# Kernel tuning notes

Hardware: AMD Instinct MI355X
Metric: run time of the kernel (lower is better)

The kernel has to match this reference:

```python
import jax, jax.numpy as jnp
import numpy as np

B, HG, WG, D, NH, K = 4, 32, 32, 768, 12, 7
HD = D // NH  # 64


def _neigh_idx(H, W, k):
    # NATTEN semantics: 7x7 window centered at the query, shifted (clamped)
    # at borders so every query has exactly k*k neighbors.
    si = np.clip(np.arange(H) - k // 2, 0, H - k)  # [H] window row starts
    sj = np.clip(np.arange(W) - k // 2, 0, W - k)  # [W] window col starts
    ri = si[:, None] + np.arange(k)[None, :]       # [H, k]
    cj = sj[:, None] + np.arange(k)[None, :]       # [W, k]
    idx = ri[:, None, :, None] * W + cj[None, :, None, :]  # [H, W, k, k]
    return jnp.asarray(idx.reshape(H * W, k * k), dtype=jnp.int32)


def setup_inputs() -> dict:
    key = jax.random.key(0)
    ks = jax.random.split(key, 3)
    s = D ** -0.5
    return {
        "x": jax.random.normal(ks[0], (B, HG * WG, D), dtype=jnp.float32),
        "qkv_w": jax.random.normal(ks[1], (3 * D, D), dtype=jnp.float32) * s,
        "qkv_b": jnp.zeros((3 * D,), dtype=jnp.float32),
        "proj_w": jax.random.normal(ks[2], (D, D), dtype=jnp.float32) * s,
        "proj_b": jnp.zeros((D,), dtype=jnp.float32),
    }


def reference(x, qkv_w, qkv_b, proj_w, proj_b):
    b, n, d = x.shape  # n == HG*WG
    idx = _neigh_idx(HG, WG, K)  # [n, K*K] flat neighbor token indices

    qkv = x @ qkv_w.T + qkv_b                      # [b, n, 3d]
    q, k, v = jnp.split(qkv, 3, axis=-1)
    q = q.reshape(b, n, NH, HD) * (HD ** -0.5)     # [b, n, h, hd]
    k = k.reshape(b, n, NH, HD)
    v = v.reshape(b, n, NH, HD)

    kn = jnp.take(k, idx, axis=1)                  # [b, n, 49, h, hd]
    vn = jnp.take(v, idx, axis=1)                  # [b, n, 49, h, hd]

    scores = jnp.einsum('bnhd,bnkhd->bnhk', q, kn)  # [b, n, h, 49]
    attn = jax.nn.softmax(scores, axis=-1)
    out = jnp.einsum('bnhk,bnkhd->bnhd', attn, vn).reshape(b, n, d)
    return out @ proj_w.T + proj_b
```

## Files before the change

### kernel.cpp

```cpp
#include <hip/hip_runtime.h>


typedef __bf16 bf16x8 __attribute__((ext_vector_type(8)));
typedef short s16x4 __attribute__((ext_vector_type(4)));
typedef float f32x4 __attribute__((ext_vector_type(4)));

__device__ __forceinline__ unsigned short f2bf(float f) {
  unsigned u = __float_as_uint(f);
  u += 0x7fffu + ((u >> 16) & 1u);
  return (unsigned short)(u >> 16);
}

template <typename T>
__device__ __forceinline__ void gld_lds16(const T* g, T* l) {
  __builtin_amdgcn_global_load_lds((const __attribute__((address_space(1))) void*)g,
                                   (__attribute__((address_space(3))) void*)l, 16, 0, 0);
}

__global__ void cvt_kernel(const float* __restrict__ x, const float* __restrict__ w1,
                           const float* __restrict__ w2, unsigned short* __restrict__ xo,
                           unsigned short* __restrict__ w1o, unsigned short* __restrict__ w2o) {
  const int n1 = 4096 * 768 / 4;
  const int n2 = 2304 * 768 / 4;
  const int n3 = 768 * 768 / 4;
  int i = blockIdx.x * 256 + threadIdx.x;
  float4 v;
  unsigned short* dst;
  int o;
  if (i < n1) {
    o = i; v = ((const float4*)x)[o]; dst = xo;
  } else if (i < n1 + n2) {
    o = i - n1; v = ((const float4*)w1)[o]; dst = w1o;
  } else if (i < n1 + n2 + n3) {
    o = i - n1 - n2; v = ((const float4*)w2)[o]; dst = w2o;
  } else {
    return;
  }
  ushort4 r;
  r.x = f2bf(v.x); r.y = f2bf(v.y); r.z = f2bf(v.z); r.w = f2bf(v.w);
  ((ushort4*)dst)[o] = r;
}

template <int NT, int MODE>
__global__ __launch_bounds__(256) void gemm_bt(const unsigned short* __restrict__ A,
                                               const unsigned short* __restrict__ Bm,
                                               const float* __restrict__ bias,
                                               unsigned short* __restrict__ obf,
                                               unsigned short* __restrict__ vtout,
                                               float* __restrict__ of32,
                                               int N) {
  constexpr int KD = 768;
  constexpr int SBW = NT / 2;
  __shared__ __align__(16) unsigned short sA[64 * 32];
  __shared__ __align__(16) unsigned short sB[NT * 32 * 32];
  const int tid = threadIdx.x, lane = tid & 63, wv = tid >> 6;
  const int lr = lane & 15, lq = lane >> 4;
  const int m0 = blockIdx.y * 64;
  const int n0 = blockIdx.x * (NT * 32);

  const unsigned short* pA = A + (size_t)(m0 + wv * 16 + lr) * KD + lq * 8;
  const unsigned short* pB[SBW];
#pragma unroll
  for (int j = 0; j < SBW; ++j)
    pB[j] = Bm + (size_t)(n0 + (wv * SBW + j) * 16 + lr) * KD + lq * 8;

  f32x4 acc[2][NT] = {};

  for (int k0 = 0; k0 < KD; k0 += 32) {
    gld_lds16(pA + k0, sA + tid * 8);
#pragma unroll
    for (int j = 0; j < SBW; ++j)
      gld_lds16(pB[j] + k0, sB + (wv * SBW + j) * 512 + lane * 8);
    __syncthreads();

    bf16x8 af[2], bfb[NT];
#pragma unroll
    for (int im = 0; im < 2; ++im)
      af[im] = *(const bf16x8*)(sA + ((wv >> 1) * 2 + im) * 512 + lq * 128 + lr * 8);
#pragma unroll
    for (int in = 0; in < NT; ++in)
      bfb[in] = *(const bf16x8*)(sB + ((wv & 1) * NT + in) * 512 + lq * 128 + lr * 8);
#pragma unroll
    for (int im = 0; im < 2; ++im)
#pragma unroll
      for (int in = 0; in < NT; ++in)
        acc[im][in] = __builtin_amdgcn_mfma_f32_16x16x32_bf16(af[im], bfb[in], acc[im][in], 0, 0, 0);
    __syncthreads();
  }

  const int mw = m0 + (wv >> 1) * 32;
  const int nw = n0 + (wv & 1) * (NT * 16);
#pragma unroll
  for (int im = 0; im < 2; ++im) {
#pragma unroll
    for (int in = 0; in < NT; ++in) {
      int gn = nw + in * 16 + lr;
      float bsv = bias[gn];
      if (MODE == 0) {
        int sidx = gn / 768;
        int rem = gn - sidx * 768;
        int hh = rem >> 6, dd = gn & 63;
        if (sidx == 2) {
          int gm0 = mw + im * 16 + lq * 4;
          ushort4 pk;
          pk.x = f2bf(acc[im][in][0] + bsv);
          pk.y = f2bf(acc[im][in][1] + bsv);
          pk.z = f2bf(acc[im][in][2] + bsv);
          pk.w = f2bf(acc[im][in][3] + bsv);
          *(ushort4*)(vtout + (size_t)(hh * 64 + dd) * 4096 + gm0) = pk;
        } else {
          const float scale = (sidx == 0) ? 0.18033688f : 1.0f;
#pragma unroll
          for (int r = 0; r < 4; ++r) {
            int gm = mw + im * 16 + lq * 4 + r;
            obf[((size_t)(sidx * 12 + hh) * 4096 + gm) * 64 + dd] = f2bf((acc[im][in][r] + bsv) * scale);
          }
        }
      } else {
#pragma unroll
        for (int r = 0; r < 4; ++r) {
          int gm = mw + im * 16 + lq * 4 + r;
          of32[(size_t)gm * N + gn] = acc[im][in][r] + bsv;
        }
      }
    }
  }
}

__global__ __launch_bounds__(256, 2) void natten_kernel(const unsigned short* __restrict__ qkvt,
                                                        unsigned short* __restrict__ aout) {
  __shared__ __align__(16) unsigned short sQ[64 * 64];
  __shared__ __align__(16) unsigned short sK[256 * 64];
  __shared__ __align__(16) unsigned short sVt[64 * 256];
  const int h = blockIdx.x, ip = blockIdx.y, b = blockIdx.z;
  const int i0 = ip * 2;
  const int tid = threadIdx.x, lane = tid & 63, wv = tid >> 6;
  const int lg = lane >> 4, lm = lane & 15;
  int si0 = i0 - 3; si0 = si0 < 0 ? 0 : si0; if (si0 > 25) si0 = 25;
  const int gb = b * 1024;
  const unsigned short* Qg = qkvt + ((size_t)h * 4096 + gb + i0 * 32) * 64;
  const unsigned short* Kg = qkvt + ((size_t)(12 + h) * 4096 + gb) * 64;
  const unsigned short* Vg = qkvt + (size_t)24 * 4096 * 64 + (size_t)h * 64 * 4096 + gb;

#pragma unroll
  for (int it = 0; it < 2; ++it) {
    int f = it * 256 + tid;
    int q = f >> 3, c16 = f & 7;
    uint4 v = *(const uint4*)(Qg + q * 64 + c16 * 8);
    int s = q & 15;
    *(uint2*)(sQ + q * 64 + ((((c16 << 1)) ^ s) << 2)) = make_uint2(v.x, v.y);
    *(uint2*)(sQ + q * 64 + ((((c16 << 1) | 1) ^ s) << 2)) = make_uint2(v.z, v.w);
  }
#pragma unroll
  for (int it = 0; it < 8; ++it) {
    int f = it * 256 + tid;
    int t = f >> 3, c16 = f & 7;
    int wr = t >> 5, c = t & 31;
    int row = si0 + wr; if (row > 31) row = 31;
    uint4 v = *(const uint4*)(Kg + (row * 32 + c) * 64 + c16 * 8);
    int s = t & 15;
    *(uint2*)(sK + t * 64 + ((((c16 << 1)) ^ s) << 2)) = make_uint2(v.x, v.y);
    *(uint2*)(sK + t * 64 + ((((c16 << 1) | 1) ^ s) << 2)) = make_uint2(v.z, v.w);
  }
#pragma unroll
  for (int it = 0; it < 8; ++it) {
    int f = it * 256 + tid;
    int d = f >> 5, tc16 = f & 31;
    int wr = tc16 >> 2;
    int row = si0 + wr; if (row > 31) row = 31;
    uint4 v = *(const uint4*)(Vg + (size_t)d * 4096 + row * 32 + (tc16 & 3) * 8);
    int s = d & 15;
    *(uint2*)(sVt + d * 256 + ((((tc16 << 1)) ^ s) << 2)) = make_uint2(v.x, v.y);
    *(uint2*)(sVt + d * 256 + ((((tc16 << 1) | 1) ^ s) << 2)) = make_uint2(v.z, v.w);
  }
  __syncthreads();

  const int row_sel = wv >> 1;
  const int jhalf = wv & 1;
  const int i = i0 + row_sel;
  int si_w = i - 3; si_w = si_w < 0 ? 0 : si_w; if (si_w > 25) si_w = 25;
  const int toff = (si_w - si0) * 32;
  const int j = jhalf * 16 + lm;
  int sj = j - 3; sj = sj < 0 ? 0 : sj; if (sj > 25) sj = 25;

  float madd[2][4];
#pragma unroll
  for (int p = 0; p < 2; ++p)
#pragma unroll
    for (int r = 0; r < 4; ++r) {
      int c = p * 16 + lg * 4 + r;
      madd[p][r] = (c >= sj && c <= sj + 6) ? 0.f : -1e30f;
    }

  s16x4 qf[4];
  const int qrow = row_sel * 32 + j;
#pragma unroll
  for (int ks = 0; ks < 4; ++ks)
    qf[ks] = *(const s16x4*)(sQ + qrow * 64 + ((((ks << 2) + lg) ^ (qrow & 15)) << 2));

  f32x4 accS[14];
#pragma unroll
  for (int tt = 0; tt < 14; ++tt) {
    f32x4 a = {0.f, 0.f, 0.f, 0.f};
    const int trow = toff + tt * 16 + lm;
    const unsigned short* kr = sK + trow * 64;
    const int sw = trow & 15;
#pragma unroll
    for (int ks = 0; ks < 4; ++ks) {
      s16x4 kf = *(const s16x4*)(kr + ((((ks << 2) + lg) ^ sw) << 2));
      a = __builtin_amdgcn_mfma_f32_16x16x16bf16_1k(kf, qf[ks], a, 0, 0, 0);
    }
    accS[tt] = a;
  }

  float mx = -3e38f;
#pragma unroll
  for (int tt = 0; tt < 14; ++tt)
#pragma unroll
    for (int r = 0; r < 4; ++r) {
      float v = accS[tt][r] + madd[tt & 1][r];
      accS[tt][r] = v;
      mx = fmaxf(mx, v);
    }
  mx = fmaxf(mx, __shfl_xor(mx, 16, 64));
  mx = fmaxf(mx, __shfl_xor(mx, 32, 64));
  float sum = 0.f;
#pragma unroll
  for (int tt = 0; tt < 14; ++tt)
#pragma unroll
    for (int r = 0; r < 4; ++r) {
      float p = exp2f(accS[tt][r] - mx);
      accS[tt][r] = p;
      sum += p;
    }
  sum += __shfl_xor(sum, 16, 64);
  sum += __shfl_xor(sum, 32, 64);
  const float inv = 1.f / sum;

  s16x4 pf[14];
#pragma unroll
  for (int tt = 0; tt < 14; ++tt) {
    union { unsigned u[2]; s16x4 v; } pk;
    pk.u[0] = ((unsigned)f2bf(accS[tt][1]) << 16) | f2bf(accS[tt][0]);
    pk.u[1] = ((unsigned)f2bf(accS[tt][3]) << 16) | f2bf(accS[tt][2]);
    pf[tt] = pk.v;
  }

  f32x4 accO[4] = {};
  const int choff = toff >> 2;
#pragma unroll
  for (int tt = 0; tt < 14; ++tt) {
    const int c8 = choff + tt * 4 + lg;
#pragma unroll
    for (int nt = 0; nt < 4; ++nt) {
      const int d = nt * 16 + lm;
      s16x4 vf = *(const s16x4*)(sVt + d * 256 + ((c8 ^ (d & 15)) << 2));
      accO[nt] = __builtin_amdgcn_mfma_f32_16x16x16bf16_1k(pf[tt], vf, accO[nt], 0, 0, 0);
    }
  }

  float invr[4];
#pragma unroll
  for (int r = 0; r < 4; ++r) invr[r] = __shfl(inv, lg * 4 + r, 64);

  const int tokbase = gb + i * 32 + jhalf * 16;
#pragma unroll
  for (int nt = 0; nt < 4; ++nt)
#pragma unroll
    for (int r = 0; r < 4; ++r) {
      int tok = tokbase + lg * 4 + r;
      aout[(size_t)tok * 768 + h * 64 + nt * 16 + lm] = f2bf(accO[nt][r] * invr[r]);
    }
}

extern "C" void kernel_launch(void* const* d_in, const int* in_sizes, int n_in,
                              void* d_out, int out_size, void* d_ws, size_t ws_size,
                              hipStream_t stream) {
  const float* x      = (const float*)d_in[0];
  const float* qkv_w  = (const float*)d_in[1];
  const float* qkv_b  = (const float*)d_in[2];
  const float* proj_w = (const float*)d_in[3];
  const float* proj_b = (const float*)d_in[4];
  char* ws = (char*)d_ws;

  unsigned short* xb    = (unsigned short*)(ws);
  unsigned short* wqkv  = (unsigned short*)(ws + 6291456);
  unsigned short* wproj = (unsigned short*)(ws + 9830400);
  unsigned short* qkvt  = (unsigned short*)(ws + 11010048);
  unsigned short* attnb = (unsigned short*)(ws + 29884416);
  unsigned short* vt    = qkvt + (size_t)24 * 4096 * 64;
  float* out = (float*)d_out;

  cvt_kernel<<<5376, 256, 0, stream>>>(x, qkv_w, proj_w, xb, wqkv, wproj);
  gemm_bt<4, 0><<<dim3(18, 64), 256, 0, stream>>>(xb, wqkv, qkv_b, qkvt, vt, nullptr, 2304);
  natten_kernel<<<dim3(12, 16, 4), 256, 0, stream>>>(qkvt, attnb);
  gemm_bt<2, 1><<<dim3(12, 64), 256, 0, stream>>>(attnb, wproj, proj_b, nullptr, nullptr, out, 768);
}
```

Baseline: 163.9 us.

## Double-buffer GEMM LDS tiles with async global-to-LDS prefetch and wider K step

Replaces the single-buffered GEMM with a double-buffered pipeline. Each iteration now covers a K step of 64, and the tiles for iteration it+2 are issued through global_load_lds while the MFMAs of the current tile run, using explicit vmcnt/lgkmcnt waits and raw barriers. The projection GEMM also switches from a 64-wide to a 128-wide N tile, so it launches half as many blocks. This aims to hide global load latency and cut the barrier count, in exchange for more LDS per block and a hand-coded waitcnt scheme that is fragile.

```diff
diff --git a/kernel.cpp b/kernel.cpp
--- a/kernel.cpp
+++ b/kernel.cpp
@@ -16,6 +16,10 @@
   __builtin_amdgcn_global_load_lds((const __attribute__((address_space(1))) void*)g,
                                    (__attribute__((address_space(3))) void*)l, 16, 0, 0);
 }
+
+#define WAIT_VM6   __builtin_amdgcn_s_waitcnt(0x0F76)
+#define WAIT_VM0   __builtin_amdgcn_s_waitcnt(0x0F70)
+#define WAIT_LGKM0 __builtin_amdgcn_s_waitcnt(0xC07F)
 
 __global__ void cvt_kernel(const float* __restrict__ x, const float* __restrict__ w1,
                            const float* __restrict__ w2, unsigned short* __restrict__ xo,
@@ -41,59 +45,83 @@
   ((ushort4*)dst)[o] = r;
 }
 
-template <int NT, int MODE>
-__global__ __launch_bounds__(256) void gemm_bt(const unsigned short* __restrict__ A,
-                                               const unsigned short* __restrict__ Bm,
-                                               const float* __restrict__ bias,
-                                               unsigned short* __restrict__ obf,
-                                               unsigned short* __restrict__ vtout,
-                                               float* __restrict__ of32,
-                                               int N) {
-  constexpr int KD = 768;
-  constexpr int SBW = NT / 2;
-  __shared__ __align__(16) unsigned short sA[64 * 32];
-  __shared__ __align__(16) unsigned short sB[NT * 32 * 32];
+template <int MODE>
+__global__ __launch_bounds__(256) void gemm_pipe(const unsigned short* __restrict__ A,
+                                                 const unsigned short* __restrict__ Bm,
+                                                 const float* __restrict__ bias,
+                                                 unsigned short* __restrict__ obf,
+                                                 unsigned short* __restrict__ vtout,
+                                                 float* __restrict__ of32,
+                                                 int N) {
+  constexpr int KD = 768, NITER = 12;
+  __shared__ __align__(16) unsigned short sA[2 * 4096];
+  __shared__ __align__(16) unsigned short sB[2 * 8192];
   const int tid = threadIdx.x, lane = tid & 63, wv = tid >> 6;
   const int lr = lane & 15, lq = lane >> 4;
-  const int m0 = blockIdx.y * 64;
-  const int n0 = blockIdx.x * (NT * 32);
-
-  const unsigned short* pA = A + (size_t)(m0 + wv * 16 + lr) * KD + lq * 8;
-  const unsigned short* pB[SBW];
-#pragma unroll
-  for (int j = 0; j < SBW; ++j)
-    pB[j] = Bm + (size_t)(n0 + (wv * SBW + j) * 16 + lr) * KD + lq * 8;
-
-  f32x4 acc[2][NT] = {};
-
-  for (int k0 = 0; k0 < KD; k0 += 32) {
-    gld_lds16(pA + k0, sA + tid * 8);
-#pragma unroll
-    for (int j = 0; j < SBW; ++j)
-      gld_lds16(pB[j] + k0, sB + (wv * SBW + j) * 512 + lane * 8);
-    __syncthreads();
-
-    bf16x8 af[2], bfb[NT];
-#pragma unroll
-    for (int im = 0; im < 2; ++im)
-      af[im] = *(const bf16x8*)(sA + ((wv >> 1) * 2 + im) * 512 + lq * 128 + lr * 8);
-#pragma unroll
-    for (int in = 0; in < NT; ++in)
-      bfb[in] = *(const bf16x8*)(sB + ((wv & 1) * NT + in) * 512 + lq * 128 + lr * 8);
-#pragma unroll
-    for (int im = 0; im < 2; ++im)
-#pragma unroll
-      for (int in = 0; in < NT; ++in)
-        acc[im][in] = __builtin_amdgcn_mfma_f32_16x16x32_bf16(af[im], bfb[in], acc[im][in], 0, 0, 0);
-    __syncthreads();
+  const int m0 = blockIdx.y * 64, n0 = blockIdx.x * 128;
+
+  const unsigned short* gA  = A  + (size_t)(m0 + wv * 16 + lr) * KD + lq * 8;
+  const unsigned short* gB0 = Bm + (size_t)(n0 + (wv * 2) * 16 + lr) * KD + lq * 8;
+  const unsigned short* gB1 = Bm + (size_t)(n0 + (wv * 2 + 1) * 16 + lr) * KD + lq * 8;
+  unsigned short* lA  = sA + wv * 1024 + lane * 8;
+  unsigned short* lB0 = sB + (wv * 2) * 1024 + lane * 8;
+  unsigned short* lB1 = sB + (wv * 2 + 1) * 1024 + lane * 8;
+
+  auto stage = [&](int it, int bsel) {
+    const int k0 = it * 64;
+    gld_lds16(gA + k0,       lA + bsel * 4096);
+    gld_lds16(gA + k0 + 32,  lA + bsel * 4096 + 512);
+    gld_lds16(gB0 + k0,      lB0 + bsel * 8192);
+    gld_lds16(gB0 + k0 + 32, lB0 + bsel * 8192 + 512);
+    gld_lds16(gB1 + k0,      lB1 + bsel * 8192);
+    gld_lds16(gB1 + k0 + 32, lB1 + bsel * 8192 + 512);
+  };
+
+  f32x4 acc[2][4] = {};
+
+  stage(0, 0);
+  stage(1, 1);
+  WAIT_VM6;
+  __builtin_amdgcn_s_barrier();
+
+#pragma unroll
+  for (int it = 0; it < NITER; ++it) {
+    const int cur = it & 1;
+    const unsigned short* bA = sA + cur * 4096 + ((wv >> 1) * 2) * 1024 + lq * 128 + lr * 8;
+    const unsigned short* bB = sB + cur * 8192 + ((wv & 1) * 4) * 1024 + lq * 128 + lr * 8;
+    bf16x8 af[2][2], bfb[2][4];
+#pragma unroll
+    for (int c = 0; c < 2; ++c) {
+#pragma unroll
+      for (int im = 0; im < 2; ++im)
+        af[c][im] = *(const bf16x8*)(bA + im * 1024 + c * 512);
+#pragma unroll
+      for (int in = 0; in < 4; ++in)
+        bfb[c][in] = *(const bf16x8*)(bB + in * 1024 + c * 512);
+    }
+    WAIT_LGKM0;
+    __builtin_amdgcn_s_barrier();
+    if (it + 2 < NITER) stage(it + 2, cur);
+#pragma unroll
+    for (int c = 0; c < 2; ++c)
+#pragma unroll
+      for (int im = 0; im < 2; ++im)
+#pragma unroll
+        for (int in = 0; in < 4; ++in)
+          acc[im][in] = __builtin_amdgcn_mfma_f32_16x16x32_bf16(af[c][im], bfb[c][in], acc[im][in], 0, 0, 0);
+    if (it + 1 < NITER) {
+      if (it + 2 < NITER) WAIT_VM6;
+      else                WAIT_VM0;
+      __builtin_amdgcn_s_barrier();
+    }
   }
 
   const int mw = m0 + (wv >> 1) * 32;
-  const int nw = n0 + (wv & 1) * (NT * 16);
+  const int nw = n0 + (wv & 1) * 64;
 #pragma unroll
   for (int im = 0; im < 2; ++im) {
 #pragma unroll
-    for (int in = 0; in < NT; ++in) {
+    for (int in = 0; in < 4; ++in) {
       int gn = nw + in * 16 + lr;
       float bsv = bias[gn];
       if (MODE == 0) {
@@ -292,7 +320,7 @@
   float* out = (float*)d_out;
 
   cvt_kernel<<<5376, 256, 0, stream>>>(x, qkv_w, proj_w, xb, wqkv, wproj);
-  gemm_bt<4, 0><<<dim3(18, 64), 256, 0, stream>>>(xb, wqkv, qkv_b, qkvt, vt, nullptr, 2304);
+  gemm_pipe<0><<<dim3(18, 64), 256, 0, stream>>>(xb, wqkv, qkv_b, qkvt, vt, nullptr, 2304);
   natten_kernel<<<dim3(12, 16, 4), 256, 0, stream>>>(qkvt, attnb);
-  gemm_bt<2, 1><<<dim3(12, 64), 256, 0, stream>>>(attnb, wproj, proj_b, nullptr, nullptr, out, 768);
-}
+  gemm_pipe<1><<<dim3(6, 64), 256, 0, stream>>>(attnb, wproj, proj_b, nullptr, nullptr, out, 768);
+}
```

After: 156.8 us. -4.3%, faster.
